# Kernel tuning notes

Measured on AMD Instinct MI355X. Metric: run time of the kernel, lower is better.

The kernel has to match this reference:

```python
import jax, jax.numpy as jnp
import numpy as np

N_HEADS = 16

@jax.checkpoint
def feature_fn(x, neurons, weights):
    # x [B,S,D], neurons [N,D,R], weights [B,S,N] -> h [B,S,R]
    all_h = jnp.einsum('bsd,ndr->bsnr', x, neurons)
    return jnp.einsum('bsnr,bsn->bsr', all_h, weights)

@jax.checkpoint
def restore_fn(h, neurons, weights):
    # h [B,S,R], neurons [N,R,D], weights [B,S,N] -> out [B,S,D]
    all_out = jnp.einsum('bsr,nrd->bsnd', h, neurons)
    return jnp.einsum('bsnd,bsn->bsd', all_out, weights)


def setup_inputs() -> dict:
    key = jax.random.key(0)
    ks = jax.random.split(key, 12)
    B, S, D, R, N = 2, 2048, 1024, 128, 8
    inp = {
        'x': jax.random.normal(ks[0], (B, S, D), jnp.float32),
        'f_qk_neurons': jax.random.normal(ks[1], (N, D, R), jnp.float32) * 0.02,
        'f_v_neurons': jax.random.normal(ks[2], (N, D, R), jnp.float32) * 0.02,
        'r_qk_neurons': jax.random.normal(ks[3], (N, R, D), jnp.float32) * 0.02,
        'r_v_neurons': jax.random.normal(ks[4], (N, R, D), jnp.float32) * 0.02,
        'fqk_weights_Q': jax.random.uniform(ks[5], (B, S, N), jnp.float32),
        'fqk_weights_K': jax.random.uniform(ks[6], (B, S, N), jnp.float32),
        'fv_weights': jax.random.uniform(ks[7], (B, S, N), jnp.float32),
        'rqk_weights_Q': jax.random.uniform(ks[8], (B, S, N), jnp.float32),
        'rqk_weights_K': jax.random.uniform(ks[9], (B, S, N), jnp.float32),
        'rv_weights': jax.random.uniform(ks[10], (B, S, N), jnp.float32),
        'W_O': jax.random.normal(ks[11], (D, D), jnp.float32) * 0.02,
    }
    return inp


def reference(x, f_qk_neurons, f_v_neurons, r_qk_neurons, r_v_neurons,
              fqk_weights_Q, fqk_weights_K, fv_weights,
              rqk_weights_Q, rqk_weights_K, rv_weights, W_O):
    B, S, D = x.shape
    H = N_HEADS
    d_head = D // H
    # neuron-mixture feature projections (shared QK pool)
    h_q = feature_fn(x, f_qk_neurons, fqk_weights_Q)
    h_k = feature_fn(x, f_qk_neurons, fqk_weights_K)
    h_v = feature_fn(x, f_v_neurons, fv_weights)
    # neuron-mixture restore projections
    Q = restore_fn(h_q, r_qk_neurons, rqk_weights_Q)
    K = restore_fn(h_k, r_qk_neurons, rqk_weights_K)
    V = restore_fn(h_v, r_v_neurons, rv_weights)
    # split heads: [B,S,D] -> [B,H,S,d_head]
    Q = Q.reshape(B, S, H, d_head).transpose(0, 2, 1, 3)
    K = K.reshape(B, S, H, d_head).transpose(0, 2, 1, 3)
    V = V.reshape(B, S, H, d_head).transpose(0, 2, 1, 3)
    scale = jnp.sqrt(jnp.float32(d_head))
    scores = jnp.einsum('bhsd,bhtd->bhst', Q, K) / scale
    causal_mask = jnp.tril(jnp.ones((S, S), dtype=jnp.bool_))
    scores = jnp.where(causal_mask, scores, jnp.finfo(scores.dtype).min)
    attn = jax.nn.softmax(scores, axis=-1)
    attn_out = jnp.einsum('bhst,bhtd->bhsd', attn, V)
    attn_out = attn_out.transpose(0, 2, 1, 3).reshape(B, S, D)
    return attn_out @ W_O
```

## Files before the change

### kernel.cpp

```cpp
#include <hip/hip_runtime.h>
#include <stdint.h>

typedef __attribute__((ext_vector_type(8))) __bf16 bf16x8;
typedef __attribute__((ext_vector_type(4))) float f32x4;
typedef __attribute__((ext_vector_type(4))) unsigned short us4;
typedef __attribute__((ext_vector_type(8))) unsigned short us8v;

__device__ __forceinline__ unsigned short f2b(float f){
  unsigned int u = __builtin_bit_cast(unsigned int, f);
  unsigned int r = (u + 0x7fffu + ((u >> 16) & 1u)) >> 16;
  return (unsigned short)r;
}
__device__ __forceinline__ unsigned short f2b_fast(float f){
  unsigned int u = __builtin_bit_cast(unsigned int, f);
  return (unsigned short)((u + 0x8000u) >> 16);
}
__device__ __forceinline__ float b2f(unsigned short h){
  unsigned int u = ((unsigned int)h) << 16;
  return __builtin_bit_cast(float, u);
}

#define KDIM 1024
#define NDIM 1024

__global__ __launch_bounds__(256) void k_prep(
    const float* __restrict__ x,   unsigned short* __restrict__ Xbf,
    const float* __restrict__ fqk, unsigned short* __restrict__ FqkT,
    const float* __restrict__ fv,  unsigned short* __restrict__ FvT,
    const float* __restrict__ rqk, unsigned short* __restrict__ RqkT,
    const float* __restrict__ rv,  unsigned short* __restrict__ RvT,
    const float* __restrict__ wo,  unsigned short* __restrict__ WOT)
{
  __shared__ float tile[32][33];
  int blk = blockIdx.x;
  int tid = threadIdx.x;
  if (blk < 4096){
    int idx = blk * 256 + tid;
    float4 v = ((const float4*)x)[idx];
    us4 o; o.x = f2b(v.x); o.y = f2b(v.y); o.z = f2b(v.z); o.w = f2b(v.w);
    ((us4*)Xbf)[idx] = o;
    return;
  }
  int t = blk - 4096;
  int mid = t >> 10;
  int within = t & 1023;
  const float* src; unsigned short* dst;
  int b, R, C, tr, tc;
  if (mid < 2){
    src = mid == 0 ? fqk : fv;  dst = mid == 0 ? FqkT : FvT;
    R = 1024; C = 128;
    b = within >> 7; int tw = within & 127; tr = tw >> 2; tc = tw & 3;
  } else {
    src = mid == 2 ? rqk : (mid == 3 ? rv : wo);
    dst = mid == 2 ? RqkT : (mid == 3 ? RvT : WOT);
    R = 1024; C = 1024;
    b = 0; tr = within >> 5; tc = within & 31;
  }
  int r = tid >> 3, c0 = (tid & 7) * 4;
  size_t base = (size_t)b * R * C;
  float4 v = *(const float4*)&src[base + (size_t)(tr*32 + r) * C + tc*32 + c0];
  tile[r][c0+0] = v.x; tile[r][c0+1] = v.y; tile[r][c0+2] = v.z; tile[r][c0+3] = v.w;
  __syncthreads();
  us4 o;
  o.x = f2b(tile[c0+0][r]); o.y = f2b(tile[c0+1][r]);
  o.z = f2b(tile[c0+2][r]); o.w = f2b(tile[c0+3][r]);
  *(us4*)&dst[base + (size_t)(tc*32 + r) * R + tr*32 + c0] = o;
}

__global__ __launch_bounds__(128) void k_mix(const unsigned short* __restrict__ ahqk,
    const unsigned short* __restrict__ ahv,
    const float* __restrict__ fwq, const float* __restrict__ fwk, const float* __restrict__ fwv,
    const float* __restrict__ rwq, const float* __restrict__ rwk, const float* __restrict__ rwv,
    unsigned short* __restrict__ gq, unsigned short* __restrict__ gk, unsigned short* __restrict__ gv){
  int bs = blockIdx.x; int r = threadIdx.x;
  const unsigned short* aq = ahqk + (size_t)bs * 1024;
  const unsigned short* av = ahv  + (size_t)bs * 1024;
  float hq = 0.f, hk = 0.f, hv = 0.f;
  float fq[8], fk[8], fvv[8], rq[8], rk[8], rvv[8];
  #pragma unroll
  for (int n = 0; n < 8; n++){
    fq[n] = fwq[bs*8+n]; fk[n] = fwk[bs*8+n]; fvv[n] = fwv[bs*8+n];
    rq[n] = rwq[bs*8+n]; rk[n] = rwk[bs*8+n]; rvv[n] = rwv[bs*8+n];
  }
  #pragma unroll
  for (int n = 0; n < 8; n++){
    float a = b2f(aq[n*128 + r]); hq += a * fq[n]; hk += a * fk[n];
    hv += b2f(av[n*128 + r]) * fvv[n];
  }
  #pragma unroll
  for (int n = 0; n < 8; n++){
    gq[(size_t)bs*1024 + n*128 + r] = f2b(rq[n] * hq);
    gk[(size_t)bs*1024 + n*128 + r] = f2b(rk[n] * hk);
    gv[(size_t)bs*1024 + n*128 + r] = f2b(rvv[n] * hv);
  }
}

__global__ __launch_bounds__(256) void k_transpose_v(const unsigned short* __restrict__ Vp,
                                                     unsigned short* __restrict__ Vt){
  __shared__ unsigned short tile[32][36];
  int blk = blockIdx.x;
  int bh = blk >> 7, rem = blk & 127;
  int t = rem >> 3, tl = rem & 7, ts = tl >> 1, td = tl & 1;
  int tid = threadIdx.x;
  int r = tid >> 3, c0 = (tid & 7) * 4;
  us4 v = *(const us4*)&Vp[((size_t)(bh*2048 + t*128 + ts*32 + r)) * 64 + td*32 + c0];
  *(us4*)&tile[r][c0] = v;
  __syncthreads();
  us4 o;
  o.x = tile[c0+0][r]; o.y = tile[c0+1][r]; o.z = tile[c0+2][r]; o.w = tile[c0+3][r];
  *(us4*)&Vt[((size_t)((bh*16 + t)*64 + td*32 + r)) * 128 + ts*32 + c0] = o;
}


__device__ __forceinline__ void load_lds16(const void* g, void* l){
  __builtin_amdgcn_global_load_lds((const __attribute__((address_space(1))) unsigned int*)g,
                                   (__attribute__((address_space(3))) unsigned int*)l, 16, 0, 0);
}

template<int OUT_MODE, int BN>
__global__ __launch_bounds__(256) void k_gemm_bt3(
    const unsigned short* __restrict__ A0, const unsigned short* __restrict__ B0, void* __restrict__ C0,
    const unsigned short* __restrict__ A1, const unsigned short* __restrict__ B1, void* __restrict__ C1,
    const unsigned short* __restrict__ A2, const unsigned short* __restrict__ B2, void* __restrict__ C2)
{
  __shared__ unsigned short Al[2][128*32];
  __shared__ unsigned short Bl[2][BN*32];
  int nb8 = gridDim.x >> 3;
  int swz = (blockIdx.x & 7) * nb8 + (blockIdx.x >> 3);
  int job, bid;
  if constexpr (BN == 64){ job = 0; bid = swz; }
  else { job = swz >> 8; bid = swz & 255; }
  const unsigned short* A  = job == 0 ? A0 : (job == 1 ? A1 : A2);
  const unsigned short* Bt = job == 0 ? B0 : (job == 1 ? B1 : B2);
  void* C = job == 0 ? C0 : (job == 1 ? C1 : C2);
  int bx, by;
  if constexpr (BN == 64){ bx = bid & 15; by = bid >> 4; }
  else { bx = bid & 7; by = bid >> 3; }
  int m0 = by * 128, n0 = bx * BN;
  int tid = threadIdx.x, wid = tid >> 6, lane = tid & 63, l15 = lane & 15, g = lane >> 4;
  int wr = wid >> 1, wc = wid & 1;
  constexpr int WCN = BN / 2;
  constexpr int NACC = WCN / 16;

  auto stage = [&](int buf, int kt){
    #pragma unroll
    for (int i = 0; i < 2; i++){
      int c = i * 256 + tid;
      load_lds16(A + (size_t)(m0 + (c >> 2)) * KDIM + kt * 32 + (c & 3) * 8,
                 &Al[buf][(i * 256 + wid * 64) * 8]);
    }
    #pragma unroll
    for (int i = 0; i < BN/64; i++){
      int c = i * 256 + tid;
      load_lds16(Bt + (size_t)(n0 + (c >> 2)) * KDIM + kt * 32 + (c & 3) * 8,
                 &Bl[buf][(i * 256 + wid * 64) * 8]);
    }
  };

  f32x4 acc[4][NACC] = {};

  stage(0, 0);
  __syncthreads();
  int cur = 0;
  const int nk = KDIM / 32;
  for (int kt = 0; kt < nk; ++kt){
    if (kt + 1 < nk) stage(cur ^ 1, kt + 1);
    bf16x8 af[4], bfv[NACC];
    #pragma unroll
    for (int mi = 0; mi < 4; mi++)
      af[mi] = *(const bf16x8*)&Al[cur][(wr*64 + mi*16 + l15) * 32 + g * 8];
    #pragma unroll
    for (int ni = 0; ni < NACC; ni++)
      bfv[ni] = *(const bf16x8*)&Bl[cur][(wc*WCN + ni*16 + l15) * 32 + g * 8];
    #pragma unroll
    for (int mi = 0; mi < 4; mi++)
      #pragma unroll
      for (int ni = 0; ni < NACC; ni++)
        acc[mi][ni] = __builtin_amdgcn_mfma_f32_16x16x32_bf16(af[mi], bfv[ni], acc[mi][ni], 0, 0, 0);
    __syncthreads();
    cur ^= 1;
  }

  #pragma unroll
  for (int mi = 0; mi < 4; mi++){
    #pragma unroll
    for (int reg = 0; reg < 4; reg++){
      int row = m0 + wr*64 + mi*16 + g*4 + reg;
      #pragma unroll
      for (int ni = 0; ni < NACC; ni++){
        int col = n0 + wc*WCN + ni*16 + l15;
        float v = acc[mi][ni][reg];
        if (OUT_MODE == 0){
          ((float*)C)[(size_t)row * NDIM + col] = v;
        } else if (OUT_MODE == 1){
          ((unsigned short*)C)[(size_t)row * NDIM + col] = f2b(v);
        } else {
          int b = row >> 11, s = row & 2047, h = col >> 6, dh = col & 63;
          ((unsigned short*)C)[(((size_t)(b*16 + h)) * 2048 + s) * 64 + dh] = f2b(v);
        }
      }
    }
  }
}

#define PSTR 72
__global__ __launch_bounds__(512) void k_attn(
    const unsigned short* __restrict__ Qp_, const unsigned short* __restrict__ Kp_,
    const unsigned short* __restrict__ Vt, unsigned short* __restrict__ AO,
    float* __restrict__ Pws)
{
  __shared__ unsigned short Klds[2][4096];
  __shared__ unsigned short Vlds[2][4096];
  __shared__ unsigned short Plds[8][32*PSTR];

  int xb = (blockIdx.x & 7) * 60 + (blockIdx.x >> 3);
  int bh = xb / 15;
  int slot = xb % 15;
  int qt, c;
  if (slot < 3){ qt = slot; c = 0; }
  else if (slot < 9){ int s = slot - 3; qt = 3 + (s >> 1); c = s & 1; }
  else { int s = slot - 9; qt = 6 + (s >= 3 ? 1 : 0); c = (s >= 3) ? s - 3 : s; }
  int nc = qt < 3 ? 1 : (qt < 6 ? 2 : 3);
  int b = bh >> 4, h = bh & 15;
  int q0 = qt * 256;
  int kv_lo = c * 768;
  int kv_hi = min((c + 1) * 768, q0 + 256);
  int niter = (kv_hi - kv_lo) >> 6;

  int tid = threadIdx.x, w = tid >> 6, lane = tid & 63, l15 = lane & 15, g = lane >> 4;
  const unsigned short* Qw = Qp_ + ((size_t)bh * 2048 + q0 + w*32) * 64;
  const unsigned short* Kb = Kp_ + (size_t)bh * 2048 * 64;
  const unsigned short* Vb = Vt + (size_t)bh * 16 * 64 * 128;
  unsigned short* Pw = &Plds[w][0];

  int srow = tid >> 3, sj = tid & 7;

  bf16x8 aq[2][2];
  #pragma unroll
  for (int m = 0; m < 2; m++)
    #pragma unroll
    for (int kk = 0; kk < 2; kk++)
      aq[m][kk] = *(const bf16x8*)(Qw + (m*16 + l15)*64 + kk*32 + g*8);

  const float cs = 0.125f;
  float l_run[2][4] = {};
  f32x4 acc_o[2][4] = {};

  us8v kA, vA, kB, vB;

  auto issue = [&](us8v& k0, us8v& v0, int kv0){
    k0 = *(const us8v*)(Kb + ((size_t)(kv0 + srow)) * 64 + sj*8);
    int t128 = kv0 >> 7, koff = kv0 & 64;
    v0 = *(const us8v*)(Vb + ((size_t)(t128*64 + srow)) * 128 + koff + sj*8);
  };
  auto put = [&](int buf, us8v k0, us8v v0){
    *(us8v*)&Klds[buf][(sj*64 + srow)*8] = k0;
    *(us8v*)&Vlds[buf][(sj*64 + srow)*8] = v0;
  };
  auto compute = [&](int buf, int kv0){
    f32x4 s[2][4] = {};
    __builtin_amdgcn_s_setprio(1);
    #pragma unroll
    for (int ti = 0; ti < 4; ti++){
      #pragma unroll
      for (int kk = 0; kk < 2; kk++){
        bf16x8 kf = *(const bf16x8*)&Klds[buf][((kk*4 + g)*64 + ti*16 + l15)*8];
        s[0][ti] = __builtin_amdgcn_mfma_f32_16x16x32_bf16(aq[0][kk], kf, s[0][ti], 0, 0, 0);
        s[1][ti] = __builtin_amdgcn_mfma_f32_16x16x32_bf16(aq[1][kk], kf, s[1][ti], 0, 0, 0);
      }
    }
    __builtin_amdgcn_s_setprio(0);
    bool partial = (kv0 + 64 > q0);
    #pragma unroll
    for (int m = 0; m < 2; m++){
      #pragma unroll
      for (int reg = 0; reg < 4; reg++){
        int row = q0 + w*32 + m*16 + g*4 + reg;
        #pragma unroll
        for (int ti = 0; ti < 4; ti++){
          float x = s[m][ti][reg] * cs;
          if (partial){
            int col = kv0 + ti*16 + l15;
            if (col > row) x = -1e30f;
          }
          float p = __expf(x);
          l_run[m][reg] += p;
          Pw[(m*16 + g*4 + reg)*PSTR + ((ti ^ g)*16) + l15] = f2b_fast(p);
        }
      }
    }
    bf16x8 pa[2][2];
    #pragma unroll
    for (int m = 0; m < 2; m++)
      #pragma unroll
      for (int cc = 0; cc < 2; cc++){
        int tiL = cc*2 + (g >> 1);
        int tiS = tiL ^ ((l15 >> 2) & 3);
        pa[m][cc] = *(const bf16x8*)&Pw[(m*16 + l15)*PSTR + tiS*16 + (g & 1)*8];
      }
    __builtin_amdgcn_s_setprio(1);
    #pragma unroll
    for (int ni = 0; ni < 4; ni++){
      #pragma unroll
      for (int cc = 0; cc < 2; cc++){
        bf16x8 vf = *(const bf16x8*)&Vlds[buf][((cc*4 + g)*64 + ni*16 + l15)*8];
        acc_o[0][ni] = __builtin_amdgcn_mfma_f32_16x16x32_bf16(pa[0][cc], vf, acc_o[0][ni], 0, 0, 0);
        acc_o[1][ni] = __builtin_amdgcn_mfma_f32_16x16x32_bf16(pa[1][cc], vf, acc_o[1][ni], 0, 0, 0);
      }
    }
    __builtin_amdgcn_s_setprio(0);
  };

  issue(kA, vA, kv_lo);
  put(0, kA, vA);
  __syncthreads();
  int it = 0, cur = 0;
  while (true){
    if (it + 1 < niter) issue(kB, vB, kv_lo + (it+1)*64);
    compute(cur, kv_lo + it*64);
    if (it + 1 < niter) put(cur ^ 1, kB, vB);
    __syncthreads();
    cur ^= 1; ++it;
    if (it >= niter) break;
    if (it + 1 < niter) issue(kA, vA, kv_lo + (it+1)*64);
    compute(cur, kv_lo + it*64);
    if (it + 1 < niter) put(cur ^ 1, kA, vA);
    __syncthreads();
    cur ^= 1; ++it;
    if (it >= niter) break;
  }

  #pragma unroll
  for (int m = 0; m < 2; m++)
    #pragma unroll
    for (int reg = 0; reg < 4; reg++){
      #pragma unroll
      for (int off = 1; off < 16; off <<= 1) l_run[m][reg] += __shfl_xor(l_run[m][reg], off);
    }

  if (nc == 1){
    #pragma unroll
    for (int m = 0; m < 2; m++)
      #pragma unroll
      for (int ni = 0; ni < 4; ni++)
        #pragma unroll
        for (int reg = 0; reg < 4; reg++){
          int row = q0 + w*32 + m*16 + g*4 + reg;
          int dh = ni*16 + l15;
          AO[((size_t)(b*2048 + row)) * 1024 + h*64 + dh] = f2b(acc_o[m][ni][reg] / l_run[m][reg]);
        }
  } else {
    float* P0 = Pws + ((size_t)((bh*5 + (qt - 3))*3 + c)) * (256*65);
    #pragma unroll
    for (int m = 0; m < 2; m++)
      #pragma unroll
      for (int ni = 0; ni < 4; ni++)
        #pragma unroll
        for (int reg = 0; reg < 4; reg++){
          int lrow = w*32 + m*16 + g*4 + reg;
          P0[lrow*64 + ni*16 + l15] = acc_o[m][ni][reg];
        }
    if (l15 == 0){
      #pragma unroll
      for (int m = 0; m < 2; m++)
        #pragma unroll
        for (int reg = 0; reg < 4; reg++){
          int lrow = w*32 + m*16 + g*4 + reg;
          P0[256*64 + lrow] = l_run[m][reg];
        }
    }
  }
}

__global__ __launch_bounds__(256) void k_attn_reduce(const float* __restrict__ Pws,
                                                     unsigned short* __restrict__ AO){
  int blk = blockIdx.x;
  int bh = blk / 5, qtp = blk % 5, qt = 3 + qtp;
  int b = bh >> 4, h = bh & 15;
  int nc = qtp < 3 ? 2 : 3;
  const size_t stride = 256*65;
  const float* base = Pws + ((size_t)(bh*5 + qtp)*3) * stride;
  int tid = threadIdx.x;
  #pragma unroll 4
  for (int i = 0; i < 64; i++){
    int idx = i*256 + tid;
    int row = idx >> 6, d = idx & 63;
    float l = base[stride*0 + 256*64 + row] + base[stride*1 + 256*64 + row];
    float o = base[stride*0 + idx] + base[stride*1 + idx];
    if (nc == 3){
      l += base[stride*2 + 256*64 + row];
      o += base[stride*2 + idx];
    }
    AO[((size_t)(b*2048 + qt*256 + row)) * 1024 + h*64 + d] = f2b(o / l);
  }
}


extern "C" void kernel_launch(void* const* d_in, const int* in_sizes, int n_in,
                              void* d_out, int out_size, void* d_ws, size_t ws_size,
                              hipStream_t stream){
  const float* x    = (const float*)d_in[0];
  const float* fqk  = (const float*)d_in[1];
  const float* fv   = (const float*)d_in[2];
  const float* rqk  = (const float*)d_in[3];
  const float* rv   = (const float*)d_in[4];
  const float* fwQ  = (const float*)d_in[5];
  const float* fwK  = (const float*)d_in[6];
  const float* fwV  = (const float*)d_in[7];
  const float* rwQ  = (const float*)d_in[8];
  const float* rwK  = (const float*)d_in[9];
  const float* rwV  = (const float*)d_in[10];
  const float* wo   = (const float*)d_in[11];
  float* out = (float*)d_out;

  char* ws = (char*)d_ws;
  size_t off = 0;
  auto alloc = [&](size_t bytes)->void*{
    void* p = ws + off; off += (bytes + 255) & ~(size_t)255; return p;
  };
  unsigned short* FqkT = (unsigned short*)alloc(1024ull*1024*2);
  unsigned short* FvT  = (unsigned short*)alloc(1024ull*1024*2);
  unsigned short* RqkT = (unsigned short*)alloc(1024ull*1024*2);
  unsigned short* RvT  = (unsigned short*)alloc(1024ull*1024*2);
  unsigned short* WOT  = (unsigned short*)alloc(1024ull*1024*2);
  char* overlay = ws + off;
  unsigned short* Xbf  = (unsigned short*)alloc(4096ull*1024*2);
  unsigned short* AHqk = (unsigned short*)alloc(4096ull*1024*2);
  unsigned short* AHv  = (unsigned short*)alloc(4096ull*1024*2);
  unsigned short* Gq   = (unsigned short*)alloc(4096ull*1024*2);
  unsigned short* Gk   = (unsigned short*)alloc(4096ull*1024*2);
  unsigned short* Gv   = (unsigned short*)alloc(4096ull*1024*2);
  unsigned short* Qp   = (unsigned short*)alloc(4096ull*1024*2);
  unsigned short* Kp   = (unsigned short*)alloc(4096ull*1024*2);
  unsigned short* Vpk  = (unsigned short*)alloc(4096ull*1024*2);
  unsigned short* Vtl  = (unsigned short*)alloc(32ull*16*64*128*2);
  unsigned short* AOm  = (unsigned short*)alloc(4096ull*1024*2);
  float* Pws = (float*)overlay;

  k_prep<<<9216, 256, 0, stream>>>(x, Xbf, fqk, FqkT, fv, FvT, rqk, RqkT, rv, RvT, wo, WOT);

  k_gemm_bt3<1,128><<<512, 256, 0, stream>>>(Xbf, FqkT, AHqk, Xbf, FvT, AHv,
                                             nullptr, nullptr, nullptr);
  k_mix<<<4096, 128, 0, stream>>>(AHqk, AHv, fwQ, fwK, fwV, rwQ, rwK, rwV, Gq, Gk, Gv);
  k_gemm_bt3<2,128><<<768, 256, 0, stream>>>(Gq, RqkT, Qp, Gk, RqkT, Kp, Gv, RvT, Vpk);
  k_transpose_v<<<4096, 256, 0, stream>>>(Vpk, Vtl);
  k_attn<<<480, 512, 0, stream>>>(Qp, Kp, Vtl, AOm, Pws);
  k_attn_reduce<<<160, 256, 0, stream>>>(Pws, AOm);
  k_gemm_bt3<0,64><<<512, 256, 0, stream>>>(AOm, WOT, out,
                                            nullptr, nullptr, nullptr,
                                            nullptr, nullptr, nullptr);
}
```

Before: 215.3 us.

## Merge feature GEMMs, vectorize mix kernel, single-buffer attention K/V LDS

The two feature-projection GEMMs become one GEMM with N=2048. This relies on the transposed FqkT and FvT weights sitting next to each other in the workspace, and writes one concatenated activation buffer. The mix kernel now handles 8 rows per 256-thread block with 4-wide vector loads and stores, cutting block count and scalar memory traffic. The attention kernel drops its double-buffered K/V shared memory for a single buffer with an extra barrier per iteration. That lowers LDS use, which may help occupancy, but it serializes the LDS writes against compute.

```diff
diff --git a/kernel.cpp b/kernel.cpp
--- a/kernel.cpp
+++ b/kernel.cpp
@@ -21,7 +21,6 @@
 }
 
 #define KDIM 1024
-#define NDIM 1024
 
 __global__ __launch_bounds__(256) void k_prep(
     const float* __restrict__ x,   unsigned short* __restrict__ Xbf,
@@ -67,31 +66,44 @@
   *(us4*)&dst[base + (size_t)(tc*32 + r) * R + tr*32 + c0] = o;
 }
 
-__global__ __launch_bounds__(128) void k_mix(const unsigned short* __restrict__ ahqk,
-    const unsigned short* __restrict__ ahv,
+__global__ __launch_bounds__(256) void k_mix(const unsigned short* __restrict__ AH,
     const float* __restrict__ fwq, const float* __restrict__ fwk, const float* __restrict__ fwv,
     const float* __restrict__ rwq, const float* __restrict__ rwk, const float* __restrict__ rwv,
     unsigned short* __restrict__ gq, unsigned short* __restrict__ gk, unsigned short* __restrict__ gv){
-  int bs = blockIdx.x; int r = threadIdx.x;
-  const unsigned short* aq = ahqk + (size_t)bs * 1024;
-  const unsigned short* av = ahv  + (size_t)bs * 1024;
-  float hq = 0.f, hk = 0.f, hv = 0.f;
-  float fq[8], fk[8], fvv[8], rq[8], rk[8], rvv[8];
+  int tid = threadIdx.x;
+  int lb = tid >> 5, rq = tid & 31;
+  int bs = blockIdx.x * 8 + lb;
+  const unsigned short* row = AH + (size_t)bs * 2048;
+  float fq[8], fk[8], fv8[8], rqw[8], rkw[8], rvw[8];
   #pragma unroll
   for (int n = 0; n < 8; n++){
-    fq[n] = fwq[bs*8+n]; fk[n] = fwk[bs*8+n]; fvv[n] = fwv[bs*8+n];
-    rq[n] = rwq[bs*8+n]; rk[n] = rwk[bs*8+n]; rvv[n] = rwv[bs*8+n];
-  }
+    fq[n] = fwq[bs*8+n]; fk[n] = fwk[bs*8+n]; fv8[n] = fwv[bs*8+n];
+    rqw[n] = rwq[bs*8+n]; rkw[n] = rwk[bs*8+n]; rvw[n] = rwv[bs*8+n];
+  }
+  float hq[4] = {}, hk[4] = {}, hv[4] = {};
   #pragma unroll
   for (int n = 0; n < 8; n++){
-    float a = b2f(aq[n*128 + r]); hq += a * fq[n]; hk += a * fk[n];
-    hv += b2f(av[n*128 + r]) * fvv[n];
+    us4 a = *(const us4*)&row[n*128 + rq*4];
+    us4 av = *(const us4*)&row[1024 + n*128 + rq*4];
+    #pragma unroll
+    for (int j = 0; j < 4; j++){
+      float af = b2f(a[j]);
+      hq[j] += af * fq[n]; hk[j] += af * fk[n];
+      hv[j] += b2f(av[j]) * fv8[n];
+    }
   }
   #pragma unroll
   for (int n = 0; n < 8; n++){
-    gq[(size_t)bs*1024 + n*128 + r] = f2b(rq[n] * hq);
-    gk[(size_t)bs*1024 + n*128 + r] = f2b(rk[n] * hk);
-    gv[(size_t)bs*1024 + n*128 + r] = f2b(rvv[n] * hv);
+    us4 oq, ok, ov;
+    #pragma unroll
+    for (int j = 0; j < 4; j++){
+      oq[j] = f2b(rqw[n] * hq[j]);
+      ok[j] = f2b(rkw[n] * hk[j]);
+      ov[j] = f2b(rvw[n] * hv[j]);
+    }
+    *(us4*)&gq[(size_t)bs*1024 + n*128 + rq*4] = oq;
+    *(us4*)&gk[(size_t)bs*1024 + n*128 + rq*4] = ok;
+    *(us4*)&gv[(size_t)bs*1024 + n*128 + rq*4] = ov;
   }
 }
 
@@ -117,7 +129,7 @@
                                    (__attribute__((address_space(3))) unsigned int*)l, 16, 0, 0);
 }
 
-template<int OUT_MODE, int BN>
+template<int OUT_MODE, int BN, int ND, int NTILE>
 __global__ __launch_bounds__(256) void k_gemm_bt3(
     const unsigned short* __restrict__ A0, const unsigned short* __restrict__ B0, void* __restrict__ C0,
     const unsigned short* __restrict__ A1, const unsigned short* __restrict__ B1, void* __restrict__ C1,
@@ -127,15 +139,12 @@
   __shared__ unsigned short Bl[2][BN*32];
   int nb8 = gridDim.x >> 3;
   int swz = (blockIdx.x & 7) * nb8 + (blockIdx.x >> 3);
-  int job, bid;
-  if constexpr (BN == 64){ job = 0; bid = swz; }
-  else { job = swz >> 8; bid = swz & 255; }
+  int job = swz / NTILE, bid = swz % NTILE;
   const unsigned short* A  = job == 0 ? A0 : (job == 1 ? A1 : A2);
   const unsigned short* Bt = job == 0 ? B0 : (job == 1 ? B1 : B2);
   void* C = job == 0 ? C0 : (job == 1 ? C1 : C2);
-  int bx, by;
-  if constexpr (BN == 64){ bx = bid & 15; by = bid >> 4; }
-  else { bx = bid & 7; by = bid >> 3; }
+  constexpr int NBX = ND / BN;
+  int bx = bid % NBX, by = bid / NBX;
   int m0 = by * 128, n0 = bx * BN;
   int tid = threadIdx.x, wid = tid >> 6, lane = tid & 63, l15 = lane & 15, g = lane >> 4;
   int wr = wid >> 1, wc = wid & 1;
@@ -191,9 +200,9 @@
         int col = n0 + wc*WCN + ni*16 + l15;
         float v = acc[mi][ni][reg];
         if (OUT_MODE == 0){
-          ((float*)C)[(size_t)row * NDIM + col] = v;
+          ((float*)C)[(size_t)row * ND + col] = v;
         } else if (OUT_MODE == 1){
-          ((unsigned short*)C)[(size_t)row * NDIM + col] = f2b(v);
+          ((unsigned short*)C)[(size_t)row * ND + col] = f2b(v);
         } else {
           int b = row >> 11, s = row & 2047, h = col >> 6, dh = col & 63;
           ((unsigned short*)C)[(((size_t)(b*16 + h)) * 2048 + s) * 64 + dh] = f2b(v);
@@ -209,8 +218,8 @@
     const unsigned short* __restrict__ Vt, unsigned short* __restrict__ AO,
     float* __restrict__ Pws)
 {
-  __shared__ unsigned short Klds[2][4096];
-  __shared__ unsigned short Vlds[2][4096];
+  __shared__ unsigned short Klds[4096];
+  __shared__ unsigned short Vlds[4096];
   __shared__ unsigned short Plds[8][32*PSTR];
 
   int xb = (blockIdx.x & 7) * 60 + (blockIdx.x >> 3);
@@ -253,18 +262,18 @@
     int t128 = kv0 >> 7, koff = kv0 & 64;
     v0 = *(const us8v*)(Vb + ((size_t)(t128*64 + srow)) * 128 + koff + sj*8);
   };
-  auto put = [&](int buf, us8v k0, us8v v0){
-    *(us8v*)&Klds[buf][(sj*64 + srow)*8] = k0;
-    *(us8v*)&Vlds[buf][(sj*64 + srow)*8] = v0;
+  auto put = [&](us8v k0, us8v v0){
+    *(us8v*)&Klds[(sj*64 + srow)*8] = k0;
+    *(us8v*)&Vlds[(sj*64 + srow)*8] = v0;
   };
-  auto compute = [&](int buf, int kv0){
+  auto compute = [&](int kv0){
     f32x4 s[2][4] = {};
     __builtin_amdgcn_s_setprio(1);
     #pragma unroll
     for (int ti = 0; ti < 4; ti++){
       #pragma unroll
       for (int kk = 0; kk < 2; kk++){
-        bf16x8 kf = *(const bf16x8*)&Klds[buf][((kk*4 + g)*64 + ti*16 + l15)*8];
+        bf16x8 kf = *(const bf16x8*)&Klds[((kk*4 + g)*64 + ti*16 + l15)*8];
         s[0][ti] = __builtin_amdgcn_mfma_f32_16x16x32_bf16(aq[0][kk], kf, s[0][ti], 0, 0, 0);
         s[1][ti] = __builtin_amdgcn_mfma_f32_16x16x32_bf16(aq[1][kk], kf, s[1][ti], 0, 0, 0);
       }
@@ -303,7 +312,7 @@
     for (int ni = 0; ni < 4; ni++){
       #pragma unroll
       for (int cc = 0; cc < 2; cc++){
-        bf16x8 vf = *(const bf16x8*)&Vlds[buf][((cc*4 + g)*64 + ni*16 + l15)*8];
+        bf16x8 vf = *(const bf16x8*)&Vlds[((cc*4 + g)*64 + ni*16 + l15)*8];
         acc_o[0][ni] = __builtin_amdgcn_mfma_f32_16x16x32_bf16(pa[0][cc], vf, acc_o[0][ni], 0, 0, 0);
         acc_o[1][ni] = __builtin_amdgcn_mfma_f32_16x16x32_bf16(pa[1][cc], vf, acc_o[1][ni], 0, 0, 0);
       }
@@ -312,22 +321,27 @@
   };
 
   issue(kA, vA, kv_lo);
-  put(0, kA, vA);
+  put(kA, vA);
   __syncthreads();
-  int it = 0, cur = 0;
+  int it = 0;
   while (true){
-    if (it + 1 < niter) issue(kB, vB, kv_lo + (it+1)*64);
-    compute(cur, kv_lo + it*64);
-    if (it + 1 < niter) put(cur ^ 1, kB, vB);
+    bool more = (it + 1 < niter);
+    if (more) issue(kB, vB, kv_lo + (it+1)*64);
+    compute(kv_lo + it*64);
+    ++it;
+    if (!more) break;
     __syncthreads();
-    cur ^= 1; ++it;
-    if (it >= niter) break;
-    if (it + 1 < niter) issue(kA, vA, kv_lo + (it+1)*64);
-    compute(cur, kv_lo + it*64);
-    if (it + 1 < niter) put(cur ^ 1, kA, vA);
+    put(kB, vB);
     __syncthreads();
-    cur ^= 1; ++it;
-    if (it >= niter) break;
+
+    more = (it + 1 < niter);
+    if (more) issue(kA, vA, kv_lo + (it+1)*64);
+    compute(kv_lo + it*64);
+    ++it;
+    if (!more) break;
+    __syncthreads();
+    put(kA, vA);
+    __syncthreads();
   }
 
   #pragma unroll
@@ -425,8 +439,7 @@
   unsigned short* WOT  = (unsigned short*)alloc(1024ull*1024*2);
   char* overlay = ws + off;
   unsigned short* Xbf  = (unsigned short*)alloc(4096ull*1024*2);
-  unsigned short* AHqk = (unsigned short*)alloc(4096ull*1024*2);
-  unsigned short* AHv  = (unsigned short*)alloc(4096ull*1024*2);
+  unsigned short* AHc  = (unsigned short*)alloc(4096ull*2048*2);
   unsigned short* Gq   = (unsigned short*)alloc(4096ull*1024*2);
   unsigned short* Gk   = (unsigned short*)alloc(4096ull*1024*2);
   unsigned short* Gv   = (unsigned short*)alloc(4096ull*1024*2);
@@ -439,14 +452,15 @@
 
   k_prep<<<9216, 256, 0, stream>>>(x, Xbf, fqk, FqkT, fv, FvT, rqk, RqkT, rv, RvT, wo, WOT);
 
-  k_gemm_bt3<1,128><<<512, 256, 0, stream>>>(Xbf, FqkT, AHqk, Xbf, FvT, AHv,
-                                             nullptr, nullptr, nullptr);
-  k_mix<<<4096, 128, 0, stream>>>(AHqk, AHv, fwQ, fwK, fwV, rwQ, rwK, rwV, Gq, Gk, Gv);
-  k_gemm_bt3<2,128><<<768, 256, 0, stream>>>(Gq, RqkT, Qp, Gk, RqkT, Kp, Gv, RvT, Vpk);
+  k_gemm_bt3<1,128,2048,512><<<512, 256, 0, stream>>>(Xbf, FqkT, AHc,
+                                                      nullptr, nullptr, nullptr,
+                                                      nullptr, nullptr, nullptr);
+  k_mix<<<512, 256, 0, stream>>>(AHc, fwQ, fwK, fwV, rwQ, rwK, rwV, Gq, Gk, Gv);
+  k_gemm_bt3<2,128,1024,256><<<768, 256, 0, stream>>>(Gq, RqkT, Qp, Gk, RqkT, Kp, Gv, RvT, Vpk);
   k_transpose_v<<<4096, 256, 0, stream>>>(Vpk, Vtl);
   k_attn<<<480, 512, 0, stream>>>(Qp, Kp, Vtl, AOm, Pws);
   k_attn_reduce<<<160, 256, 0, stream>>>(Pws, AOm);
-  k_gemm_bt3<0,64><<<512, 256, 0, stream>>>(AOm, WOT, out,
-                                            nullptr, nullptr, nullptr,
-                                            nullptr, nullptr, nullptr);
-}
+  k_gemm_bt3<0,64,1024,512><<<512, 256, 0, stream>>>(AOm, WOT, out,
+                                                     nullptr, nullptr, nullptr,
+                                                     nullptr, nullptr, nullptr);
+}
```

New measurement: 217.4 us. Within noise of the previous version (+1.0%).
